# Performance work log

Measured on AMD Instinct MI355X. Metric: run time of the kernel, lower is better.

Reference implementation:

```python
import jax, jax.numpy as jnp
import numpy as np

TEMPERATURE = 0.2
NUMBER_CLASSES = 1000
LOSS_SCALE = 0.001

N, F = 8192, 256
M = 20000
DEPTH = 4


def setup_inputs() -> dict:
    key = jax.random.key(0)
    k1, k2, k3, k4 = jax.random.split(key, 4)
    gt_labels = jax.random.randint(k1, (N,), 0, NUMBER_CLASSES, dtype=jnp.int32)
    box_features = jax.random.normal(k2, (N, F), dtype=jnp.float32)
    memory = jax.random.normal(k3, (M, F), dtype=jnp.float32)
    trace_idx = jax.random.randint(k4, (NUMBER_CLASSES, DEPTH), 0, M, dtype=jnp.int32)
    return {"gt_labels": gt_labels, "box_features": box_features,
            "memory": memory, "trace_idx": trace_idx}


def reference(gt_labels, box_features, memory, trace_idx):
    # logits[i, j] = dot(f_i, m_j) / T  (the nested python loops fused into one GEMM)
    logits = jnp.einsum('nf,mf->nm', box_features, memory) / TEMPERATURE  # [N, M]
    # fenmu = sum_j exp(logits)  ->  log(fenmu) = logsumexp
    lse = jax.nn.logsumexp(logits, axis=-1)  # [N]
    # gather the trace entries for each item's label: [N, DEPTH]
    traces = trace_idx[gt_labels]  # [N, DEPTH]
    sel = jnp.take_along_axis(logits, traces, axis=1)  # [N, DEPTH]
    depth_w = jnp.arange(DEPTH, dtype=logits.dtype)  # gj = depth
    sum_gj = depth_w.sum()  # sum of layer weights (0+1+2+3)
    # per item: -sum_d gj * log(sim_d / fenmu) / sum_gj
    per_item = -jnp.sum((sel - lse[:, None]) * depth_w, axis=-1) / sum_gj  # [N]
    # background filter: items with label == number_classes contribute nothing
    fg = (gt_labels != NUMBER_CLASSES)
    loss = jnp.sum(jnp.where(fg, per_item, 0.0)) * LOSS_SCALE
    return loss
```

## Files before the change

kernel.cpp:

```cpp
#include <hip/hip_runtime.h>
#include <hip/hip_bf16.h>
#include <stdint.h>

#define NROWS 8192
#define FDIM 256
#define MCOLS 20000
#define NT32 625
#define MSPLIT 16
#define NCLS 1000
#define LOG2E 1.44269504088896f
#define LN2   0.69314718055994f


typedef short short8 __attribute__((ext_vector_type(8)));
typedef float f32x4 __attribute__((ext_vector_type(4)));

typedef __attribute__((address_space(3))) unsigned int lds_u32;
typedef const __attribute__((address_space(1))) unsigned int glb_u32;

__device__ __forceinline__ float ex2(float x) {
    float r;
    asm("v_exp_f32 %0, %1" : "=v"(r) : "v"(x));
    return r;
}

__device__ __forceinline__ unsigned short f2bf(float x) {
    unsigned u = __float_as_uint(x);
    unsigned r = (u + 0x7FFFu + ((u >> 16) & 1u)) >> 16;
    return (unsigned short)r;
}

__global__ void conv_kernel(const float* __restrict__ in, unsigned short* __restrict__ out,
                            int n4, float scale) {
    int idx = blockIdx.x * blockDim.x + threadIdx.x;
    if (idx >= n4) return;
    float4 v = ((const float4*)in)[idx];
    ushort4 o;
    o.x = f2bf(v.x * scale); o.y = f2bf(v.y * scale);
    o.z = f2bf(v.z * scale); o.w = f2bf(v.w * scale);
    ((ushort4*)out)[idx] = o;
}

__global__ void sel_kernel(const int* __restrict__ gt, const float* __restrict__ F,
                           const float* __restrict__ Mem, const int* __restrict__ trace,
                           float* __restrict__ wsel) {
    int lane = threadIdx.x & 63, wid = threadIdx.x >> 6;
    int i = blockIdx.x * 4 + wid;
    int label = gt[i];
    float w = 0.0f;
    if (label >= 0 && label < NCLS) {
        float4 fv = ((const float4*)(F + (size_t)i * FDIM))[lane];
        #pragma unroll
        for (int d = 1; d <= 3; ++d) {
            int tr = trace[label * 4 + d];
            float4 mv = ((const float4*)(Mem + (size_t)tr * FDIM))[lane];
            float dot = fv.x*mv.x + fv.y*mv.y + fv.z*mv.z + fv.w*mv.w;
            #pragma unroll
            for (int off = 32; off >= 1; off >>= 1) dot += __shfl_xor(dot, off, 64);
            w += (float)d * dot;
        }
    }
    if (lane == 0) wsel[i] = w * 5.0f;
}

__global__ __launch_bounds__(256, 2) void lse_gemm(
        const unsigned short* __restrict__ Fb, const unsigned short* __restrict__ Mb,
        float* __restrict__ pm, float* __restrict__ ps) {
    __shared__ __align__(16) char smem[2 * 16384];

    const int split  = blockIdx.x;
    const int rowblk = blockIdx.y;
    const int tid  = threadIdx.x;
    const int lane = tid & 63, wid = tid >> 6;
    const int r0 = lane & 15, hi = lane >> 4;
    const int rowbase = rowblk * 128 + wid * 32;

    short8 a[2][8];
    #pragma unroll
    for (int rf = 0; rf < 2; ++rf)
        #pragma unroll
        for (int kk = 0; kk < 8; ++kk)
            a[rf][kk] = *(const short8*)(Fb + (size_t)(rowbase + rf*16 + r0) * FDIM + kk*32 + hi*8);

    float m[8], s[8];
    #pragma unroll
    for (int q = 0; q < 8; ++q) { m[q] = -3.0e38f; s[q] = 0.0f; }

    const int t0 = (split * NT32) / MSPLIT;
    const int t1 = ((split + 1) * NT32) / MSPLIT;

    int srcoff[4];
    #pragma unroll
    for (int c = 0; c < 4; ++c) {
        const int g = (wid * 4 + c) * 64 + lane;
        const int j = g >> 5, o = g & 31;
        srcoff[c] = j * 512 + ((o ^ (j & 7)) << 4);
    }

#define STAGE(buf, t)                                                              \
    do {                                                                           \
        const char* srcT = (const char*)Mb + (size_t)(t) * 16384;                  \
        _Pragma("unroll")                                                          \
        for (int c = 0; c < 4; ++c) {                                              \
            __builtin_amdgcn_global_load_lds(                                      \
                (glb_u32*)(srcT + srcoff[c]),                                      \
                (lds_u32*)((char*)smem + (buf) * 16384 + (wid * 4 + c) * 1024),    \
                16, 0, 0);                                                         \
        }                                                                          \
    } while (0)

    const int swzr = (r0 & 7) << 4;
    int roff[8];
    #pragma unroll
    for (int kk = 0; kk < 8; ++kk)
        roff[kk] = r0 * 512 + ((kk * 64 + hi * 16) ^ swzr);

#define BODY(BUF, t, pref)                                                         \
    do {                                                                           \
        if (pref) STAGE((BUF) ^ 1, (t) + 1);                                       \
        f32x4 acc00 = {0,0,0,0}, acc01 = {0,0,0,0}, acc10 = {0,0,0,0}, acc11 = {0,0,0,0}; \
        _Pragma("unroll")                                                          \
        for (int kk = 0; kk < 8; ++kk) {                                           \
            short8 b0 = *(const short8*)(smem + roff[kk] + (BUF) * 16384);         \
            short8 b1 = *(const short8*)(smem + roff[kk] + (BUF) * 16384 + 8192);  \
            acc00 = __builtin_amdgcn_mfma_f32_16x16x32_bf16(a[0][kk], b0, acc00, 0, 0, 0); \
            acc10 = __builtin_amdgcn_mfma_f32_16x16x32_bf16(a[1][kk], b0, acc10, 0, 0, 0); \
            acc01 = __builtin_amdgcn_mfma_f32_16x16x32_bf16(a[0][kk], b1, acc01, 0, 0, 0); \
            acc11 = __builtin_amdgcn_mfma_f32_16x16x32_bf16(a[1][kk], b1, acc11, 0, 0, 0); \
        }                                                                          \
        _Pragma("unroll")                                                          \
        for (int r = 0; r < 4; ++r) {                                              \
            { float v0 = acc00[r], v1 = acc01[r];                                  \
              float nm = fmaxf(fmaxf(m[r], v0), v1);                               \
              float em = ex2(m[r] - nm), e0 = ex2(v0 - nm), e1 = ex2(v1 - nm);     \
              s[r] = fmaf(s[r], em, e0 + e1); m[r] = nm; }                         \
            { float v0 = acc10[r], v1 = acc11[r];                                  \
              float nm = fmaxf(fmaxf(m[4 + r], v0), v1);                           \
              float em = ex2(m[4 + r] - nm), e0 = ex2(v0 - nm), e1 = ex2(v1 - nm); \
              s[4 + r] = fmaf(s[4 + r], em, e0 + e1); m[4 + r] = nm; }             \
        }                                                                          \
        __syncthreads();                                                           \
    } while (0)

    STAGE(0, t0);
    __syncthreads();

    int t = t0;
    while (t + 2 <= t1) {
        BODY(0, t, true);
        BODY(1, t + 1, (t + 2 < t1));
        t += 2;
    }
    if (t < t1) BODY(0, t, false);

#undef BODY
#undef STAGE

    #pragma unroll
    for (int off = 1; off <= 8; off <<= 1) {
        #pragma unroll
        for (int q = 0; q < 8; ++q) {
            float om = __shfl_xor(m[q], off, 64);
            float os = __shfl_xor(s[q], off, 64);
            float nm = fmaxf(m[q], om);
            float sn = fmaf(s[q], ex2(m[q] - nm), os * ex2(om - nm));
            m[q] = nm; s[q] = sn;
        }
    }
    if (r0 == 0) {
        #pragma unroll
        for (int rf = 0; rf < 2; ++rf)
            #pragma unroll
            for (int r = 0; r < 4; ++r) {
                int row = rowbase + rf * 16 + hi * 4 + r;
                pm[split * NROWS + row] = m[rf * 4 + r];
                ps[split * NROWS + row] = s[rf * 4 + r];
            }
    }
}

__global__ void finalize_kernel(const int* __restrict__ gt, const float* __restrict__ wsel,
                                const float* __restrict__ pm, const float* __restrict__ ps,
                                float* __restrict__ bpart) {
    int tid = threadIdx.x;
    int i = blockIdx.x * 256 + tid;
    float mv[MSPLIT];
    float M = -3.0e38f;
    #pragma unroll
    for (int k = 0; k < MSPLIT; ++k) { mv[k] = pm[k * NROWS + i]; M = fmaxf(M, mv[k]); }
    float S = 0.0f;
    #pragma unroll
    for (int k = 0; k < MSPLIT; ++k) S += ps[k * NROWS + i] * ex2(mv[k] - M);
    float lse = (M + __log2f(S)) * LN2;
    int label = gt[i];
    float per = (label >= 0 && label < NCLS) ? (lse - wsel[i] * (1.0f / 6.0f)) : 0.0f;
    #pragma unroll
    for (int off = 32; off >= 1; off >>= 1) per += __shfl_xor(per, off, 64);
    __shared__ float red[4];
    int lane = tid & 63, wid = tid >> 6;
    if (lane == 0) red[wid] = per;
    __syncthreads();
    if (tid == 0) bpart[blockIdx.x] = red[0] + red[1] + red[2] + red[3];
}

__global__ void sum_kernel(const float* __restrict__ bpart, float* __restrict__ out) {
    int tid = threadIdx.x;
    float v = (tid < 32) ? bpart[tid] : 0.0f;
    #pragma unroll
    for (int off = 32; off >= 1; off >>= 1) v += __shfl_xor(v, off, 64);
    if (tid == 0) out[0] = 0.001f * v;
}

extern "C" void kernel_launch(void* const* d_in, const int* in_sizes, int n_in,
                              void* d_out, int out_size, void* d_ws, size_t ws_size,
                              hipStream_t stream) {
    const int*   gt    = (const int*)d_in[0];
    const float* F     = (const float*)d_in[1];
    const float* Mem   = (const float*)d_in[2];
    const int*   trace = (const int*)d_in[3];
    float* out = (float*)d_out;

    char* w = (char*)d_ws;
    unsigned short* Mb = (unsigned short*)w;
    unsigned short* Fb = (unsigned short*)(w + 10240000);
    float* wsel  = (float*)(w + 14434304);
    float* pm    = (float*)(w + 14467072);
    float* ps    = (float*)(w + 14991360);
    float* bpart = (float*)(w + 15515648);

    conv_kernel<<<dim3((MCOLS * FDIM / 4) / 256), dim3(256), 0, stream>>>(Mem, Mb, MCOLS * FDIM / 4, 1.0f);
    conv_kernel<<<dim3((NROWS * FDIM / 4) / 256), dim3(256), 0, stream>>>(F, Fb, NROWS * FDIM / 4, 5.0f * LOG2E);
    sel_kernel<<<dim3(NROWS / 4), dim3(256), 0, stream>>>(gt, F, Mem, trace, wsel);
    lse_gemm<<<dim3(MSPLIT, NROWS / 128), dim3(256), 0, stream>>>(Fb, Mb, pm, ps);
    finalize_kernel<<<dim3(NROWS / 256), dim3(256), 0, stream>>>(gt, wsel, pm, ps, bpart);
    sum_kernel<<<dim3(1), dim3(64), 0, stream>>>(bpart, out);
}
```

Baseline: 113.0 us.

## Double per-wave row tile to 64 rows and raise MFMA priority

Each wave now keeps 64 rows of F in registers (4 row fragments) instead of 32, so every B fragment read from LDS feeds 8 MFMAs instead of 4. Each block covers 256 rows, which halves the grid's row blocks and the total staging of memory tiles into LDS. s_setprio is also raised around the MFMA loop. In exchange register use roughly doubles and launch bounds drop to one block per SM, and the grid shrinks to 512 blocks, which lowers occupancy and latency hiding.

```diff
diff --git a/kernel.cpp b/kernel.cpp
--- a/kernel.cpp
+++ b/kernel.cpp
@@ -63,7 +63,7 @@
     if (lane == 0) wsel[i] = w * 5.0f;
 }
 
-__global__ __launch_bounds__(256, 2) void lse_gemm(
+__global__ __launch_bounds__(256, 1) void lse_gemm(
         const unsigned short* __restrict__ Fb, const unsigned short* __restrict__ Mb,
         float* __restrict__ pm, float* __restrict__ ps) {
     __shared__ __align__(16) char smem[2 * 16384];
@@ -73,18 +73,18 @@
     const int tid  = threadIdx.x;
     const int lane = tid & 63, wid = tid >> 6;
     const int r0 = lane & 15, hi = lane >> 4;
-    const int rowbase = rowblk * 128 + wid * 32;
-
-    short8 a[2][8];
-    #pragma unroll
-    for (int rf = 0; rf < 2; ++rf)
+    const int rowbase = rowblk * 256 + wid * 64;
+
+    short8 a[4][8];
+    #pragma unroll
+    for (int rf = 0; rf < 4; ++rf)
         #pragma unroll
         for (int kk = 0; kk < 8; ++kk)
             a[rf][kk] = *(const short8*)(Fb + (size_t)(rowbase + rf*16 + r0) * FDIM + kk*32 + hi*8);
 
-    float m[8], s[8];
-    #pragma unroll
-    for (int q = 0; q < 8; ++q) { m[q] = -3.0e38f; s[q] = 0.0f; }
+    float m[16], s[16];
+    #pragma unroll
+    for (int q = 0; q < 16; ++q) { m[q] = -3.0e38f; s[q] = 0.0f; }
 
     const int t0 = (split * NT32) / MSPLIT;
     const int t1 = ((split + 1) * NT32) / MSPLIT;
@@ -118,27 +118,32 @@
 #define BODY(BUF, t, pref)                                                         \
     do {                                                                           \
         if (pref) STAGE((BUF) ^ 1, (t) + 1);                                       \
-        f32x4 acc00 = {0,0,0,0}, acc01 = {0,0,0,0}, acc10 = {0,0,0,0}, acc11 = {0,0,0,0}; \
+        f32x4 c0[4], c1[4];                                                        \
+        _Pragma("unroll")                                                          \
+        for (int rf = 0; rf < 4; ++rf) { f32x4 z = {0,0,0,0}; c0[rf] = z; c1[rf] = z; } \
+        __builtin_amdgcn_s_setprio(1);                                             \
         _Pragma("unroll")                                                          \
         for (int kk = 0; kk < 8; ++kk) {                                           \
-            short8 b0 = *(const short8*)(smem + roff[kk] + (BUF) * 16384);         \
-            short8 b1 = *(const short8*)(smem + roff[kk] + (BUF) * 16384 + 8192);  \
-            acc00 = __builtin_amdgcn_mfma_f32_16x16x32_bf16(a[0][kk], b0, acc00, 0, 0, 0); \
-            acc10 = __builtin_amdgcn_mfma_f32_16x16x32_bf16(a[1][kk], b0, acc10, 0, 0, 0); \
-            acc01 = __builtin_amdgcn_mfma_f32_16x16x32_bf16(a[0][kk], b1, acc01, 0, 0, 0); \
-            acc11 = __builtin_amdgcn_mfma_f32_16x16x32_bf16(a[1][kk], b1, acc11, 0, 0, 0); \
+            const char* bp = smem + (BUF) * 16384 + roff[kk];                      \
+            short8 b0 = *(const short8*)bp;                                        \
+            short8 b1 = *(const short8*)(bp + 8192);                               \
+            _Pragma("unroll")                                                      \
+            for (int rf = 0; rf < 4; ++rf) {                                       \
+                c0[rf] = __builtin_amdgcn_mfma_f32_16x16x32_bf16(a[rf][kk], b0, c0[rf], 0, 0, 0); \
+                c1[rf] = __builtin_amdgcn_mfma_f32_16x16x32_bf16(a[rf][kk], b1, c1[rf], 0, 0, 0); \
+            }                                                                      \
         }                                                                          \
-        _Pragma("unroll")                                                          \
-        for (int r = 0; r < 4; ++r) {                                              \
-            { float v0 = acc00[r], v1 = acc01[r];                                  \
-              float nm = fmaxf(fmaxf(m[r], v0), v1);                               \
-              float em = ex2(m[r] - nm), e0 = ex2(v0 - nm), e1 = ex2(v1 - nm);     \
-              s[r] = fmaf(s[r], em, e0 + e1); m[r] = nm; }                         \
-            { float v0 = acc10[r], v1 = acc11[r];                                  \
-              float nm = fmaxf(fmaxf(m[4 + r], v0), v1);                           \
-              float em = ex2(m[4 + r] - nm), e0 = ex2(v0 - nm), e1 = ex2(v1 - nm); \
-              s[4 + r] = fmaf(s[4 + r], em, e0 + e1); m[4 + r] = nm; }             \
-        }                                                                          \
+        __builtin_amdgcn_s_setprio(0);                                             \
+        _Pragma("unroll")                                                          \
+        for (int rf = 0; rf < 4; ++rf)                                             \
+            _Pragma("unroll")                                                      \
+            for (int r = 0; r < 4; ++r) {                                          \
+                const int q = rf * 4 + r;                                          \
+                float v0 = c0[rf][r], v1 = c1[rf][r];                              \
+                float nm = fmaxf(fmaxf(m[q], v0), v1);                             \
+                float em = ex2(m[q] - nm), e0 = ex2(v0 - nm), e1 = ex2(v1 - nm);   \
+                s[q] = fmaf(s[q], em, e0 + e1); m[q] = nm;                         \
+            }                                                                      \
         __syncthreads();                                                           \
     } while (0)
 
@@ -159,7 +164,7 @@
     #pragma unroll
     for (int off = 1; off <= 8; off <<= 1) {
         #pragma unroll
-        for (int q = 0; q < 8; ++q) {
+        for (int q = 0; q < 16; ++q) {
             float om = __shfl_xor(m[q], off, 64);
             float os = __shfl_xor(s[q], off, 64);
             float nm = fmaxf(m[q], om);
@@ -169,7 +174,7 @@
     }
     if (r0 == 0) {
         #pragma unroll
-        for (int rf = 0; rf < 2; ++rf)
+        for (int rf = 0; rf < 4; ++rf)
             #pragma unroll
             for (int r = 0; r < 4; ++r) {
                 int row = rowbase + rf * 16 + hi * 4 + r;
@@ -231,7 +236,7 @@
     conv_kernel<<<dim3((MCOLS * FDIM / 4) / 256), dim3(256), 0, stream>>>(Mem, Mb, MCOLS * FDIM / 4, 1.0f);
     conv_kernel<<<dim3((NROWS * FDIM / 4) / 256), dim3(256), 0, stream>>>(F, Fb, NROWS * FDIM / 4, 5.0f * LOG2E);
     sel_kernel<<<dim3(NROWS / 4), dim3(256), 0, stream>>>(gt, F, Mem, trace, wsel);
-    lse_gemm<<<dim3(MSPLIT, NROWS / 128), dim3(256), 0, stream>>>(Fb, Mb, pm, ps);
+    lse_gemm<<<dim3(MSPLIT, NROWS / 256), dim3(256), 0, stream>>>(Fb, Mb, pm, ps);
     finalize_kernel<<<dim3(NROWS / 256), dim3(256), 0, stream>>>(gt, wsel, pm, ps, bpart);
     sum_kernel<<<dim3(1), dim3(64), 0, stream>>>(bpart, out);
 }
```

After: 136.9 us. 21.2% more time.

## Deepen GEMM pipeline to four LDS stages with 512-thread blocks and setprio

Applied to the files above, without the earlier changes.

The fused GEMM+logsumexp kernel now uses 512-thread blocks covering 256 rows, so each staged memory tile is reused by twice as many waves. LDS buffering goes from two to four stages with a prefetch distance of two. The full __syncthreads is replaced by an explicit vmcnt wait plus s_barrier, and s_setprio is raised around the MFMA loop. The aim is to cut global-to-LDS traffic per FLOP and hide load latency better, at the cost of more LDS per block, which may limit occupancy, and more hand-managed synchronization. The epilogue store indexing in the hidden lines may also need updating for the new 256-row block mapping.

```diff
diff --git a/kernel.cpp b/kernel.cpp
--- a/kernel.cpp
+++ b/kernel.cpp
@@ -63,17 +63,17 @@
     if (lane == 0) wsel[i] = w * 5.0f;
 }
 
-__global__ __launch_bounds__(256, 2) void lse_gemm(
+__global__ __launch_bounds__(512, 4) void lse_gemm(
         const unsigned short* __restrict__ Fb, const unsigned short* __restrict__ Mb,
         float* __restrict__ pm, float* __restrict__ ps) {
-    __shared__ __align__(16) char smem[2 * 16384];
+    __shared__ __align__(16) char smem[4 * 16384];
 
     const int split  = blockIdx.x;
     const int rowblk = blockIdx.y;
     const int tid  = threadIdx.x;
     const int lane = tid & 63, wid = tid >> 6;
     const int r0 = lane & 15, hi = lane >> 4;
-    const int rowbase = rowblk * 128 + wid * 32;
+    const int rowbase = rowblk * 256 + wid * 32;
 
     short8 a[2][8];
     #pragma unroll
@@ -89,22 +89,22 @@
     const int t0 = (split * NT32) / MSPLIT;
     const int t1 = ((split + 1) * NT32) / MSPLIT;
 
-    int srcoff[4];
-    #pragma unroll
-    for (int c = 0; c < 4; ++c) {
-        const int g = (wid * 4 + c) * 64 + lane;
+    int srcoff[2];
+    #pragma unroll
+    for (int c = 0; c < 2; ++c) {
+        const int g = c * 512 + wid * 64 + lane;
         const int j = g >> 5, o = g & 31;
         srcoff[c] = j * 512 + ((o ^ (j & 7)) << 4);
     }
 
-#define STAGE(buf, t)                                                              \
+#define STAGE(BUF, t)                                                              \
     do {                                                                           \
         const char* srcT = (const char*)Mb + (size_t)(t) * 16384;                  \
         _Pragma("unroll")                                                          \
-        for (int c = 0; c < 4; ++c) {                                              \
+        for (int c = 0; c < 2; ++c) {                                              \
             __builtin_amdgcn_global_load_lds(                                      \
                 (glb_u32*)(srcT + srcoff[c]),                                      \
-                (lds_u32*)((char*)smem + (buf) * 16384 + (wid * 4 + c) * 1024),    \
+                (lds_u32*)(smem + (BUF) * 16384 + c * 8192 + wid * 1024),          \
                 16, 0, 0);                                                         \
         }                                                                          \
     } while (0)
@@ -115,45 +115,70 @@
     for (int kk = 0; kk < 8; ++kk)
         roff[kk] = r0 * 512 + ((kk * 64 + hi * 16) ^ swzr);
 
-#define BODY(BUF, t, pref)                                                         \
+#define COMPUTE(BASEPTR, t)                                                        \
     do {                                                                           \
-        if (pref) STAGE((BUF) ^ 1, (t) + 1);                                       \
-        f32x4 acc00 = {0,0,0,0}, acc01 = {0,0,0,0}, acc10 = {0,0,0,0}, acc11 = {0,0,0,0}; \
+        f32x4 c00 = {0,0,0,0}, c01 = {0,0,0,0}, c10 = {0,0,0,0}, c11 = {0,0,0,0};  \
+        __builtin_amdgcn_s_setprio(1);                                             \
         _Pragma("unroll")                                                          \
         for (int kk = 0; kk < 8; ++kk) {                                           \
-            short8 b0 = *(const short8*)(smem + roff[kk] + (BUF) * 16384);         \
-            short8 b1 = *(const short8*)(smem + roff[kk] + (BUF) * 16384 + 8192);  \
-            acc00 = __builtin_amdgcn_mfma_f32_16x16x32_bf16(a[0][kk], b0, acc00, 0, 0, 0); \
-            acc10 = __builtin_amdgcn_mfma_f32_16x16x32_bf16(a[1][kk], b0, acc10, 0, 0, 0); \
-            acc01 = __builtin_amdgcn_mfma_f32_16x16x32_bf16(a[0][kk], b1, acc01, 0, 0, 0); \
-            acc11 = __builtin_amdgcn_mfma_f32_16x16x32_bf16(a[1][kk], b1, acc11, 0, 0, 0); \
+            const char* bp = (BASEPTR) + roff[kk];                                 \
+            short8 b0 = *(const short8*)bp;                                        \
+            short8 b1 = *(const short8*)(bp + 8192);                               \
+            c00 = __builtin_amdgcn_mfma_f32_16x16x32_bf16(a[0][kk], b0, c00, 0, 0, 0); \
+            c10 = __builtin_amdgcn_mfma_f32_16x16x32_bf16(a[1][kk], b0, c10, 0, 0, 0); \
+            c01 = __builtin_amdgcn_mfma_f32_16x16x32_bf16(a[0][kk], b1, c01, 0, 0, 0); \
+            c11 = __builtin_amdgcn_mfma_f32_16x16x32_bf16(a[1][kk], b1, c11, 0, 0, 0); \
         }                                                                          \
+        __builtin_amdgcn_s_setprio(0);                                             \
         _Pragma("unroll")                                                          \
         for (int r = 0; r < 4; ++r) {                                              \
-            { float v0 = acc00[r], v1 = acc01[r];                                  \
+            { float v0 = c00[r], v1 = c01[r];                                      \
               float nm = fmaxf(fmaxf(m[r], v0), v1);                               \
               float em = ex2(m[r] - nm), e0 = ex2(v0 - nm), e1 = ex2(v1 - nm);     \
               s[r] = fmaf(s[r], em, e0 + e1); m[r] = nm; }                         \
-            { float v0 = acc10[r], v1 = acc11[r];                                  \
+            { float v0 = c10[r], v1 = c11[r];                                      \
               float nm = fmaxf(fmaxf(m[4 + r], v0), v1);                           \
               float em = ex2(m[4 + r] - nm), e0 = ex2(v0 - nm), e1 = ex2(v1 - nm); \
               s[4 + r] = fmaf(s[4 + r], em, e0 + e1); m[4 + r] = nm; }             \
         }                                                                          \
-        __syncthreads();                                                           \
     } while (0)
 
+#define BODY(BUF, t)                                                               \
+    do {                                                                           \
+        const bool pref = (t) + 2 < t1;                                            \
+        if (pref) STAGE(((BUF) + 2) & 3, (t) + 2);                                 \
+        COMPUTE(smem + (BUF) * 16384, t);                                          \
+        if (pref) { asm volatile("s_waitcnt vmcnt(2)" ::: "memory"); }             \
+        else      { asm volatile("s_waitcnt vmcnt(0)" ::: "memory"); }             \
+        __builtin_amdgcn_s_barrier();                                              \
+        __builtin_amdgcn_sched_barrier(0);                                         \
+    } while (0)
+
     STAGE(0, t0);
-    __syncthreads();
+    STAGE(1, t0 + 1);
+    asm volatile("s_waitcnt vmcnt(2)" ::: "memory");
+    __builtin_amdgcn_s_barrier();
+    __builtin_amdgcn_sched_barrier(0);
 
     int t = t0;
-    while (t + 2 <= t1) {
-        BODY(0, t, true);
-        BODY(1, t + 1, (t + 2 < t1));
-        t += 2;
-    }
-    if (t < t1) BODY(0, t, false);
+    while (t + 4 <= t1) {
+        BODY(0, t); BODY(1, t + 1); BODY(2, t + 2); BODY(3, t + 3);
+        t += 4;
+    }
+    while (t < t1) {
+        const int bufb = ((t - t0) & 3) * 16384;
+        const bool pref = t + 2 < t1;
+        if (pref) STAGE(((t - t0) + 2) & 3, t + 2);
+        COMPUTE(smem + bufb, t);
+        if (pref) { asm volatile("s_waitcnt vmcnt(2)" ::: "memory"); }
+        else      { asm volatile("s_waitcnt vmcnt(0)" ::: "memory"); }
+        __builtin_amdgcn_s_barrier();
+        __builtin_amdgcn_sched_barrier(0);
+        ++t;
+    }
 
 #undef BODY
+#undef COMPUTE
 #undef STAGE
 
     #pragma unroll
@@ -231,7 +256,7 @@
     conv_kernel<<<dim3((MCOLS * FDIM / 4) / 256), dim3(256), 0, stream>>>(Mem, Mb, MCOLS * FDIM / 4, 1.0f);
     conv_kernel<<<dim3((NROWS * FDIM / 4) / 256), dim3(256), 0, stream>>>(F, Fb, NROWS * FDIM / 4, 5.0f * LOG2E);
     sel_kernel<<<dim3(NROWS / 4), dim3(256), 0, stream>>>(gt, F, Mem, trace, wsel);
-    lse_gemm<<<dim3(MSPLIT, NROWS / 128), dim3(256), 0, stream>>>(Fb, Mb, pm, ps);
+    lse_gemm<<<dim3(MSPLIT, NROWS / 256), dim3(512), 0, stream>>>(Fb, Mb, pm, ps);
     finalize_kernel<<<dim3(NROWS / 256), dim3(256), 0, stream>>>(gt, wsel, pm, ps, bpart);
     sum_kernel<<<dim3(1), dim3(64), 0, stream>>>(bpart, out);
 }
```

Result: slower. 241.8 us (+114.1%).

## Software-pipeline MFMA tiles with online softmax using two accumulator sets

Applied to the files above, without the earlier changes.

Restructures the main loop so the MFMA GEMM for one tile runs alongside the exp/max softmax update of the previous tile, using two register accumulator sets (A/B) with a peeled prologue and epilogue. It also raises wave priority with s_setprio around the MFMA block. The aim is to hide the transcendental/VALU softmax cost behind matrix-core work. In exchange it uses more registers, which may reduce occupancy, and the loop bounds logic becomes more intricate.

```diff
diff --git a/kernel.cpp b/kernel.cpp
--- a/kernel.cpp
+++ b/kernel.cpp
@@ -22,6 +22,10 @@
     float r;
     asm("v_exp_f32 %0, %1" : "=v"(r) : "v"(x));
     return r;
+}
+
+__device__ __forceinline__ f32x4 mfma16(short8 a, short8 b, f32x4 c) {
+    return __builtin_amdgcn_mfma_f32_16x16x32_bf16(a, b, c, 0, 0, 0);
 }
 
 __device__ __forceinline__ unsigned short f2bf(float x) {
@@ -97,14 +101,14 @@
         srcoff[c] = j * 512 + ((o ^ (j & 7)) << 4);
     }
 
-#define STAGE(buf, t)                                                              \
+#define STAGE(BUF, t)                                                              \
     do {                                                                           \
         const char* srcT = (const char*)Mb + (size_t)(t) * 16384;                  \
         _Pragma("unroll")                                                          \
         for (int c = 0; c < 4; ++c) {                                              \
             __builtin_amdgcn_global_load_lds(                                      \
                 (glb_u32*)(srcT + srcoff[c]),                                      \
-                (lds_u32*)((char*)smem + (buf) * 16384 + (wid * 4 + c) * 1024),    \
+                (lds_u32*)(smem + (BUF) * 16384 + (wid * 4 + c) * 1024),           \
                 16, 0, 0);                                                         \
         }                                                                          \
     } while (0)
@@ -115,45 +119,69 @@
     for (int kk = 0; kk < 8; ++kk)
         roff[kk] = r0 * 512 + ((kk * 64 + hi * 16) ^ swzr);
 
-#define BODY(BUF, t, pref)                                                         \
+    f32x4 cA00, cA01, cA10, cA11, cB00, cB01, cB10, cB11;
+
+#define MFMA_TILE(BUF, S)                                                          \
     do {                                                                           \
-        if (pref) STAGE((BUF) ^ 1, (t) + 1);                                       \
-        f32x4 acc00 = {0,0,0,0}, acc01 = {0,0,0,0}, acc10 = {0,0,0,0}, acc11 = {0,0,0,0}; \
+        f32x4 z = {0, 0, 0, 0};                                                    \
+        c##S##00 = z; c##S##01 = z; c##S##10 = z; c##S##11 = z;                    \
+        __builtin_amdgcn_s_setprio(1);                                             \
         _Pragma("unroll")                                                          \
         for (int kk = 0; kk < 8; ++kk) {                                           \
-            short8 b0 = *(const short8*)(smem + roff[kk] + (BUF) * 16384);         \
-            short8 b1 = *(const short8*)(smem + roff[kk] + (BUF) * 16384 + 8192);  \
-            acc00 = __builtin_amdgcn_mfma_f32_16x16x32_bf16(a[0][kk], b0, acc00, 0, 0, 0); \
-            acc10 = __builtin_amdgcn_mfma_f32_16x16x32_bf16(a[1][kk], b0, acc10, 0, 0, 0); \
-            acc01 = __builtin_amdgcn_mfma_f32_16x16x32_bf16(a[0][kk], b1, acc01, 0, 0, 0); \
-            acc11 = __builtin_amdgcn_mfma_f32_16x16x32_bf16(a[1][kk], b1, acc11, 0, 0, 0); \
+            const char* bp = smem + (BUF) * 16384 + roff[kk];                      \
+            short8 b0 = *(const short8*)bp;                                        \
+            short8 b1 = *(const short8*)(bp + 8192);                               \
+            c##S##00 = mfma16(a[0][kk], b0, c##S##00);                             \
+            c##S##10 = mfma16(a[1][kk], b0, c##S##10);                             \
+            c##S##01 = mfma16(a[0][kk], b1, c##S##01);                             \
+            c##S##11 = mfma16(a[1][kk], b1, c##S##11);                             \
         }                                                                          \
+        __builtin_amdgcn_s_setprio(0);                                             \
+    } while (0)
+
+#define SOFTMAX(S)                                                                 \
+    do {                                                                           \
         _Pragma("unroll")                                                          \
         for (int r = 0; r < 4; ++r) {                                              \
-            { float v0 = acc00[r], v1 = acc01[r];                                  \
+            { float v0 = c##S##00[r], v1 = c##S##01[r];                            \
               float nm = fmaxf(fmaxf(m[r], v0), v1);                               \
               float em = ex2(m[r] - nm), e0 = ex2(v0 - nm), e1 = ex2(v1 - nm);     \
               s[r] = fmaf(s[r], em, e0 + e1); m[r] = nm; }                         \
-            { float v0 = acc10[r], v1 = acc11[r];                                  \
+            { float v0 = c##S##10[r], v1 = c##S##11[r];                            \
               float nm = fmaxf(fmaxf(m[4 + r], v0), v1);                           \
               float em = ex2(m[4 + r] - nm), e0 = ex2(v0 - nm), e1 = ex2(v1 - nm); \
               s[4 + r] = fmaf(s[4 + r], em, e0 + e1); m[4 + r] = nm; }             \
         }                                                                          \
-        __syncthreads();                                                           \
     } while (0)
 
     STAGE(0, t0);
     __syncthreads();
-
-    int t = t0;
+    STAGE(1, t0 + 1);
+    MFMA_TILE(0, A);
+    __syncthreads();
+
+    int t = t0 + 1;
     while (t + 2 <= t1) {
-        BODY(0, t, true);
-        BODY(1, t + 1, (t + 2 < t1));
+        STAGE(0, t + 1);
+        MFMA_TILE(1, B);
+        SOFTMAX(A);
+        __syncthreads();
+        if (t + 2 < t1) STAGE(1, t + 2);
+        MFMA_TILE(0, A);
+        SOFTMAX(B);
+        __syncthreads();
         t += 2;
     }
-    if (t < t1) BODY(0, t, false);
-
-#undef BODY
+    if (t < t1) {
+        MFMA_TILE(1, B);
+        SOFTMAX(A);
+        SOFTMAX(B);
+    } else {
+        SOFTMAX(A);
+    }
+
+#undef SOFTMAX
+#undef MFMA_TILE
 #undef STAGE
 
     #pragma unroll
```

Result: no change. 114.9 us (+1.7%).
